# Optimization experiments

Measured on AMD Instinct MI355X. Metric: run time of the kernel, lower is better.

## Reference

```python
import jax, jax.numpy as jnp
import numpy as np

N, IN_DIM, H1, H2 = 12288, 512, 256, 128

def setup_inputs() -> dict:
    key = jax.random.key(0)
    k = jax.random.split(key, 6)
    glorot = lambda kk, fi, fo: jax.random.normal(kk, (fi, fo), jnp.float32) * np.sqrt(2.0 / (fi + fo))
    return {
        "X": jax.random.normal(k[0], (N, IN_DIM), jnp.float32),
        "adj": jax.random.uniform(k[1], (N, N), jnp.float32) / N,  # scaled like a normalized adjacency
        "noise": jax.random.normal(k[2], (N, H2), jnp.float32),
        "W0": glorot(k[3], IN_DIM, H1),
        "W_mu": glorot(k[4], H1, H2),
        "W_logstd": glorot(k[5], H1, H2),
    }

def reference(X, adj, noise, W0, W_mu, W_logstd):
    # GraphConvSparse layer 1: relu(adj @ (X @ W0))
    hidden = jax.nn.relu(adj @ (X @ W0))            # [N, H1]
    # mean / logstd heads (identity activation)
    mean = adj @ (hidden @ W_mu)                    # [N, H2]
    logstd = adj @ (hidden @ W_logstd)              # [N, H2]
    # reparameterization
    Z = noise * jnp.exp(logstd) + mean              # [N, H2]
    # dot-product decode
    A_pred = jax.nn.sigmoid(Z @ Z.T)                # [N, N]
    return A_pred
```

## Files before the change

kernel.cpp:

```cpp
#include <hip/hip_runtime.h>
#include <hip/hip_fp8.h>
#include <stdint.h>

#define NN 12288
#define IND 512
#define H1D 256
#define H2D 128

using bf16x8 = __attribute__((ext_vector_type(8))) short;
using f32x4  = __attribute__((ext_vector_type(4))) float;
using u32x4  = __attribute__((ext_vector_type(4))) unsigned int;

__device__ __forceinline__ unsigned short f2bf(float f){
  unsigned int u = __float_as_uint(f);
  return (unsigned short)((u + 0x7fffu + ((u >> 16) & 1u)) >> 16);
}
__device__ __forceinline__ float bf2f(unsigned short h){
  return __uint_as_float(((unsigned int)h) << 16);
}
__device__ __forceinline__ void gload_lds16(const void* g, void* l){
  __builtin_amdgcn_global_load_lds(
      (const __attribute__((address_space(1))) unsigned int*)(uintptr_t)g,
      (__attribute__((address_space(3))) unsigned int*)(unsigned int)(uintptr_t)l,
      16, 0, 0);
}
template<bool HI>
__device__ __forceinline__ unsigned cvt2(float a, float b, unsigned old){
#if __has_builtin(__builtin_amdgcn_cvt_pk_fp8_f32)
  return (unsigned)__builtin_amdgcn_cvt_pk_fp8_f32(a, b, (int)old, HI);
#else
  __hip_fp8_e4m3 pa(a), pb(b);
  unsigned v = (unsigned)pa.__x | ((unsigned)pb.__x << 8);
  return HI ? ((old & 0x0000FFFFu) | (v << 16)) : ((old & 0xFFFF0000u) | v);
#endif
}
__device__ __forceinline__ void sync_v(int n){
  switch(n){
    case 0: asm volatile("s_waitcnt vmcnt(0) lgkmcnt(0)" ::: "memory"); break;
    case 1: asm volatile("s_waitcnt vmcnt(1) lgkmcnt(0)" ::: "memory"); break;
    case 4: asm volatile("s_waitcnt vmcnt(4) lgkmcnt(0)" ::: "memory"); break;
    default: asm volatile("s_waitcnt vmcnt(5) lgkmcnt(0)" ::: "memory"); break;
  }
  __builtin_amdgcn_s_barrier();
  __builtin_amdgcn_sched_barrier(0);
}

__global__ __launch_bounds__(256) void k_w0t(const float* __restrict__ W0,
                                             char* __restrict__ W0T){
  __shared__ float Ls[64][65];
  const int t = (int)threadIdx.x;
  const int k0 = (int)blockIdx.x * 64;
  const int h0 = (int)blockIdx.y * 64;
  {
    const int r = t >> 2, c = (t & 3) * 16;
    const float* p = W0 + (size_t)(k0 + r) * H1D + h0 + c;
#pragma unroll
    for (int q = 0; q < 4; ++q)
      *(float4*)&Ls[r][c + q*4] = *(const float4*)(p + q*4);
  }
  __syncthreads();
  const int h = t >> 2, kc = (t & 3) * 16;
  u32x4 pk;
#pragma unroll
  for (int q = 0; q < 4; ++q){
    unsigned wv = cvt2<false>(Ls[kc+q*4+0][h], Ls[kc+q*4+1][h], 0u);
    wv = cvt2<true>(Ls[kc+q*4+2][h], Ls[kc+q*4+3][h], wv);
    pk[q] = wv;
  }
  *(u32x4*)(W0T + (size_t)(h0 + h) * IND + k0 + kc) = pk;
}

#define GEMM_MFMA_F8(CUR) \
  { _Pragma("unroll") \
    for (int kk = 0; kk < 4; ++kk){ \
      long af[3]; long bfr[2]; \
      _Pragma("unroll") \
      for (int mi = 0; mi < 3; ++mi){ \
        int row = mi*16 + l15; \
        int off = row*128 + ((kk*32 + l16*8) ^ ((row & 7) << 4)); \
        af[mi] = *(const long*)(Alds[CUR] + off); \
      } \
      _Pragma("unroll") \
      for (int ni = 0; ni < 2; ++ni){ \
        int row = w*32 + ni*16 + l15; \
        int off = row*128 + ((kk*32 + l16*8) ^ ((row & 7) << 4)); \
        bfr[ni] = *(const long*)(Blds[CUR] + off); \
      } \
      _Pragma("unroll") \
      for (int mi = 0; mi < 3; ++mi) \
        _Pragma("unroll") \
        for (int ni = 0; ni < 2; ++ni) \
          acc[mi][ni] = __builtin_amdgcn_mfma_f32_16x16x32_fp8_fp8(af[mi], bfr[ni], acc[mi][ni], 0, 0, 0); \
    } }

#define GLDS_B(SIDX, BUF) \
  { _Pragma("unroll") \
    for (int i = 0; i < 4; ++i){ \
      int P = i*8192 + t*16; \
      int row = P >> 7; \
      int Li = (P & 127) ^ ((row & 7) << 4); \
      gload_lds16(btb + (size_t)row * btsb + kbB + (size_t)(SIDX)*128 + Li, \
                  Blds[BUF] + i*8192 + w*1024); \
    } }

#define GLDS_A(SIDX, BUF) \
  if (w < 6){ \
    gload_lds16(af8 + (size_t)(m0 + w*8 + rw8) * NN + kbase + (size_t)(SIDX)*128 + gsw, \
                Alds[BUF] + w*1024); \
  }

#define LOAD_A(Q0,Q1,Q2,Q3, SIDX) { \
  const float* p = abase + (size_t)(SIDX)*128; \
  Q0 = __builtin_nontemporal_load((const f32x4*)(p)); \
  Q1 = __builtin_nontemporal_load((const f32x4*)(p+4)); \
  Q2 = __builtin_nontemporal_load((const f32x4*)(p+8)); \
  Q3 = __builtin_nontemporal_load((const f32x4*)(p+12)); \
}

#define PACK_A(Q0,Q1,Q2,Q3, BUF, SIDX) { \
  u32x4 pk; \
  pk[0] = cvt2<false>(Q0[0]*ascale, Q0[1]*ascale, 0u); pk[0] = cvt2<true>(Q0[2]*ascale, Q0[3]*ascale, pk[0]); \
  pk[1] = cvt2<false>(Q1[0]*ascale, Q1[1]*ascale, 0u); pk[1] = cvt2<true>(Q1[2]*ascale, Q1[3]*ascale, pk[1]); \
  pk[2] = cvt2<false>(Q2[0]*ascale, Q2[1]*ascale, 0u); pk[2] = cvt2<true>(Q2[2]*ascale, Q2[3]*ascale, pk[2]); \
  pk[3] = cvt2<false>(Q3[0]*ascale, Q3[1]*ascale, 0u); pk[3] = cvt2<true>(Q3[2]*ascale, Q3[3]*ascale, pk[3]); \
  *(u32x4*)(Alds[BUF] + aoff) = pk; \
  if (DUMP) __builtin_nontemporal_store(pk, (u32x4*)(dumpP + (size_t)(m0 + ar) * NN + kbase + (size_t)(SIDX)*128 + ac)); \
}

template<int AMODE, int MODE, int DUMP>
__global__ __launch_bounds__(512, 4) void k_gemm_f8(const void* __restrict__ Ain, int lda, int K,
                                                    const char* __restrict__ Bt, int bt_stride_b,
                                                    float ascale, char* __restrict__ dumpP,
                                                    void* __restrict__ Out){
  __shared__ __align__(16) char Alds[2][48*128];
  __shared__ __align__(16) char Blds[2][256*128];
  const int t = (int)threadIdx.x;
  const int w = t >> 6, l = t & 63;
  const int l15 = l & 15, l16 = l >> 4;

  int midx, khalf;
  if (gridDim.x == 512){
    int f = (int)blockIdx.x;
    int x = f & 7;
    khalf = x >> 2;
    midx = (f >> 3) * 4 + (x & 3);
  } else { khalf = 0; midx = (int)blockIdx.x; }
  const int m0 = midx * 48;
  const int kbase = khalf * K;
  const size_t kbB = (size_t)kbase;
  const size_t btsb = (size_t)bt_stride_b;
  const char* btb = Bt;
  const int S = K >> 7;

  f32x4 acc[3][2];
#pragma unroll
  for (int mi = 0; mi < 3; ++mi)
#pragma unroll
    for (int ni = 0; ni < 2; ++ni) acc[mi][ni] = 0;

  const int ar = t >> 3, ac = (t & 7) * 16;
  const bool astage = (w < 6);
  const float* abase = (const float*)Ain + (size_t)(m0 + ar) * lda + kbase + ac;
  const int aoff = ar*128 + (ac ^ ((ar & 7) << 4));
  const char* af8 = (const char*)Ain;
  const int rw8 = l >> 3;
  const int gsw = ((l & 7) ^ rw8) << 4;

  if (AMODE == 0){
    f32x4 s0q0, s0q1, s0q2, s0q3, s1q0, s1q1, s1q2, s1q3;
    GLDS_B(0, 0);
    if (astage){
      LOAD_A(s0q0,s0q1,s0q2,s0q3, 0);
      if (S > 1) LOAD_A(s1q0,s1q1,s1q2,s1q3, 1);
      PACK_A(s0q0,s0q1,s0q2,s0q3, 0, 0);
    }
    sync_v(astage ? (DUMP ? 5 : 4) : 0);

    for (int s = 0; s < S; s += 2){
      if (s + 1 < S) GLDS_B(s + 1, 1);
      if (astage && s + 2 < S) LOAD_A(s0q0,s0q1,s0q2,s0q3, s + 2);
      GEMM_MFMA_F8(0);
      if (astage && s + 1 < S) PACK_A(s1q0,s1q1,s1q2,s1q3, 1, s + 1);
      if (s + 1 < S)
        sync_v(astage ? ((s + 2 < S) ? (DUMP ? 5 : 4) : (DUMP ? 1 : 0)) : 0);
      if (s + 1 < S){
        if (s + 2 < S) GLDS_B(s + 2, 0);
        if (astage && s + 3 < S) LOAD_A(s1q0,s1q1,s1q2,s1q3, s + 3);
        GEMM_MFMA_F8(1);
        if (astage && s + 2 < S) PACK_A(s0q0,s0q1,s0q2,s0q3, 0, s + 2);
        if (s + 2 < S)
          sync_v(astage ? ((s + 3 < S) ? (DUMP ? 5 : 4) : (DUMP ? 1 : 0)) : 0);
      }
    }
  } else {
    GLDS_B(0, 0);
    GLDS_A(0, 0);
    sync_v(0);
    for (int s = 0; s < S; ++s){
      const int cur = s & 1, nxt = cur ^ 1;
      if (s + 1 < S){ GLDS_B(s + 1, nxt); GLDS_A(s + 1, nxt); }
      if (cur == 0){ GEMM_MFMA_F8(0); } else { GEMM_MFMA_F8(1); }
      if (s + 1 < S) sync_v(0);
    }
  }

  if (MODE == 0){
    char* OutT = (char*)Out;
#pragma unroll
    for (int mi = 0; mi < 3; ++mi)
#pragma unroll
      for (int ni = 0; ni < 2; ++ni){
        int gr = m0 + mi*16 + l16*4;
        int gc = w*32 + ni*16 + l15;
        unsigned wd = cvt2<false>(acc[mi][ni][0], acc[mi][ni][1], 0u);
        wd = cvt2<true>(acc[mi][ni][2], acc[mi][ni][3], wd);
        *(unsigned*)(OutT + (size_t)gc * NN + gr) = wd;
      }
  } else {
    float* P = (float*)Out + (size_t)khalf * NN * H1D;
#pragma unroll
    for (int mi = 0; mi < 3; ++mi)
#pragma unroll
      for (int ni = 0; ni < 2; ++ni){
        int gr = m0 + mi*16 + l16*4;
        int gc = w*32 + ni*16 + l15;
#pragma unroll
        for (int v = 0; v < 4; ++v)
          P[(size_t)(gr + v) * H1D + gc] = acc[mi][ni][v];
      }
  }
}

__global__ __launch_bounds__(256) void k_combine_ht(const float* __restrict__ p0,
                                                    const float* __restrict__ p1,
                                                    char* __restrict__ HT){
  __shared__ float Ls[64][65];
  const int t = (int)threadIdx.x;
  const int n0 = (int)blockIdx.x * 64;
  const int h0 = (int)blockIdx.y * 64;
  const int lr = t >> 4, lc = (t & 15) * 4;
#pragma unroll
  for (int q = 0; q < 4; ++q){
    int n = lr + q*16;
    size_t idx = (size_t)(n0 + n) * H1D + h0 + lc;
    float4 a = *(const float4*)(p0 + idx);
    float4 b = *(const float4*)(p1 + idx);
    Ls[n][lc+0] = fmaxf(a.x + b.x, 0.f);
    Ls[n][lc+1] = fmaxf(a.y + b.y, 0.f);
    Ls[n][lc+2] = fmaxf(a.z + b.z, 0.f);
    Ls[n][lc+3] = fmaxf(a.w + b.w, 0.f);
  }
  __syncthreads();
  const int hr = t >> 2, nc = (t & 3) * 16;
  u32x4 pk;
#pragma unroll
  for (int q = 0; q < 4; ++q){
    unsigned wd = cvt2<false>(Ls[nc+q*4+0][hr], Ls[nc+q*4+1][hr], 0u);
    wd = cvt2<true>(Ls[nc+q*4+2][hr], Ls[nc+q*4+3][hr], wd);
    pk[q] = wd;
  }
  *(u32x4*)(HT + (size_t)(h0 + hr) * NN + n0 + nc) = pk;
}

__global__ __launch_bounds__(256) void k_heads(const float* __restrict__ p0,
                                               const float* __restrict__ Wmu,
                                               const float* __restrict__ Wls,
                                               const float* __restrict__ noise,
                                               unsigned short* __restrict__ Zhi,
                                               unsigned short* __restrict__ Zlo){
  __shared__ float AHs[32][256];
  __shared__ float Wms[32][128];
  __shared__ float Wlss[32][128];
  const float INV = 1.0f / 67108864.0f;
  const float* p1 = p0 + (size_t)NN * H1D;
  const int t  = (int)threadIdx.x;
  const int r0 = (int)blockIdx.x * 32;
  {
    const int r = t >> 3, c0 = (t & 7) * 32;
    size_t base = (size_t)(r0 + r) * H1D + c0;
#pragma unroll
    for (int q = 0; q < 8; ++q){
      float4 a = *(const float4*)(p0 + base + q*4);
      float4 b = *(const float4*)(p1 + base + q*4);
      AHs[r][c0 + q*4 + 0] = (a.x + b.x) * INV;
      AHs[r][c0 + q*4 + 1] = (a.y + b.y) * INV;
      AHs[r][c0 + q*4 + 2] = (a.z + b.z) * INV;
      AHs[r][c0 + q*4 + 3] = (a.w + b.w) * INV;
    }
  }
  const int j = t & 127, rg = t >> 7;
  float mu[16], ls[16];
#pragma unroll
  for (int r = 0; r < 16; ++r){ mu[r] = 0.f; ls[r] = 0.f; }

  for (int kc = 0; kc < 8; ++kc){
    __syncthreads();
    {
      const int r = t >> 3, c0 = (t & 7) * 16;
      const float* pm = Wmu + (size_t)(kc*32 + r) * H2D + c0;
      const float* pl = Wls + (size_t)(kc*32 + r) * H2D + c0;
#pragma unroll
      for (int q = 0; q < 4; ++q){
        *(float4*)&Wms[r][c0 + q*4]  = *(const float4*)(pm + q*4);
        *(float4*)&Wlss[r][c0 + q*4] = *(const float4*)(pl + q*4);
      }
    }
    __syncthreads();
#pragma unroll 4
    for (int k = 0; k < 32; ++k){
      float wm = Wms[k][j], wl = Wlss[k][j];
#pragma unroll
      for (int r = 0; r < 16; ++r){
        float a = AHs[rg*16 + r][kc*32 + k];
        mu[r] += a * wm;
        ls[r] += a * wl;
      }
    }
  }
#pragma unroll
  for (int r = 0; r < 16; ++r){
    const int i = r0 + rg*16 + r;
    float z = noise[(size_t)i * H2D + j] * __expf(ls[r]) + mu[r];
    unsigned short zh = f2bf(z);
    unsigned short zl = f2bf(z - bf2f(zh));
    Zhi[(size_t)i * H2D + j] = zh;
    Zlo[(size_t)i * H2D + j] = zl;
  }
}

__global__ __launch_bounds__(512) void k_decode(const unsigned short* __restrict__ Zhi,
                                                const unsigned short* __restrict__ Zlo,
                                                float* __restrict__ Out){
  __shared__ unsigned short T[4][128*64];
  const int t = (int)threadIdx.x;
  const int w = t >> 6, l = t & 63;
  const int l15 = l & 15, l16 = l >> 4;
  const int wr = w >> 2, wc = w & 3;
  const size_t m0 = (size_t)blockIdx.x * 128;
  const size_t n0 = (size_t)blockIdx.y * 128;

  f32x4 acc[4][2];
#pragma unroll
  for (int mi = 0; mi < 4; ++mi)
#pragma unroll
    for (int ni = 0; ni < 2; ++ni) acc[mi][ni] = 0;

#pragma unroll
  for (int p = 0; p < 2; ++p){
    if (p) __syncthreads();
#pragma unroll
    for (int i = 0; i < 2; ++i){
      int P = i*8192 + t*16;
      int row = P >> 7;
      int Li = (P & 127) ^ ((row & 7) << 4);
      size_t ga = (size_t)row * 256 + (size_t)p * 128 + Li;
      char* lb0 = (char*)T[0] + i*8192 + w*1024;
      char* lb1 = (char*)T[1] + i*8192 + w*1024;
      char* lb2 = (char*)T[2] + i*8192 + w*1024;
      char* lb3 = (char*)T[3] + i*8192 + w*1024;
      gload_lds16((const char*)Zhi + m0*256 + ga, lb0);
      gload_lds16((const char*)Zlo + m0*256 + ga, lb1);
      gload_lds16((const char*)Zhi + n0*256 + ga, lb2);
      gload_lds16((const char*)Zlo + n0*256 + ga, lb3);
    }
    __syncthreads();
#pragma unroll
    for (int kk = 0; kk < 2; ++kk){
      bf16x8 ah[4], al[4], bh[2], bl[2];
#pragma unroll
      for (int mi = 0; mi < 4; ++mi){
        int row = wr*64 + mi*16 + l15;
        int off = row*128 + ((kk*64 + l16*16) ^ ((row & 7) << 4));
        ah[mi] = *(const bf16x8*)((const char*)T[0] + off);
        al[mi] = *(const bf16x8*)((const char*)T[1] + off);
      }
#pragma unroll
      for (int ni = 0; ni < 2; ++ni){
        int row = wc*32 + ni*16 + l15;
        int off = row*128 + ((kk*64 + l16*16) ^ ((row & 7) << 4));
        bh[ni] = *(const bf16x8*)((const char*)T[2] + off);
        bl[ni] = *(const bf16x8*)((const char*)T[3] + off);
      }
#pragma unroll
      for (int mi = 0; mi < 4; ++mi)
#pragma unroll
        for (int ni = 0; ni < 2; ++ni){
          acc[mi][ni] = __builtin_amdgcn_mfma_f32_16x16x32_bf16(ah[mi], bh[ni], acc[mi][ni], 0, 0, 0);
          acc[mi][ni] = __builtin_amdgcn_mfma_f32_16x16x32_bf16(ah[mi], bl[ni], acc[mi][ni], 0, 0, 0);
          acc[mi][ni] = __builtin_amdgcn_mfma_f32_16x16x32_bf16(al[mi], bh[ni], acc[mi][ni], 0, 0, 0);
        }
    }
  }

#pragma unroll
  for (int mi = 0; mi < 4; ++mi)
#pragma unroll
    for (int ni = 0; ni < 2; ++ni){
      size_t gr = m0 + (size_t)(wr*64 + mi*16 + l16*4);
      size_t gc = n0 + (size_t)(wc*32 + ni*16 + l15);
#pragma unroll
      for (int v = 0; v < 4; ++v){
        float x = acc[mi][ni][v];
        float sg = 1.0f / (1.0f + __expf(-x));
        __builtin_nontemporal_store(sg, &Out[(gr + v) * (size_t)NN + gc]);
      }
    }
}

extern "C" void kernel_launch(void* const* d_in, const int* in_sizes, int n_in,
                              void* d_out, int out_size, void* d_ws, size_t ws_size,
                              hipStream_t stream) {
  const float* X     = (const float*)d_in[0];
  const float* adj   = (const float*)d_in[1];
  const float* noise = (const float*)d_in[2];
  const float* W0    = (const float*)d_in[3];
  const float* Wmu   = (const float*)d_in[4];
  const float* Wls   = (const float*)d_in[5];
  float* out = (float*)d_out;
  char* ws = (char*)d_ws;

  char*           XW0Tf8 = ws;
  char*           HidTf8 = ws + 3145728;
  char*           W0Tf8  = ws + 6291456;
  unsigned short* Zhi    = (unsigned short*)(ws + 6422528);
  unsigned short* Zlo    = (unsigned short*)(ws + 9568256);
  char*  adjf8 = (char*)d_out;
  float* part  = (float*)((char*)d_out + 150994944);

  const float S_ADJ = 8192.0f;

  k_w0t<<<dim3(8, 4), 256, 0, stream>>>(W0, W0Tf8);
  k_gemm_f8<0,0,0><<<256, 512, 0, stream>>>((const void*)X, IND, IND, W0Tf8, IND, 1.0f, nullptr, (void*)XW0Tf8);
  k_gemm_f8<0,1,1><<<512, 512, 0, stream>>>((const void*)adj, NN, 6144, XW0Tf8, NN, S_ADJ, adjf8, (void*)part);
  k_combine_ht<<<dim3(192, 4), 256, 0, stream>>>(part, part + (size_t)NN * H1D, HidTf8);
  k_gemm_f8<1,1,0><<<512, 512, 0, stream>>>((const void*)adjf8, NN, 6144, HidTf8, NN, 1.0f, nullptr, (void*)part);
  k_heads<<<384, 256, 0, stream>>>(part, Wmu, Wls, noise, Zhi, Zlo);
  k_decode<<<dim3(96, 96), 512, 0, stream>>>(Zhi, Zlo, out);
}
```

Before: 627.7 us.

## Split fp32-to-fp8 conversion into standalone kernels and unify GEMM into one fp8 kernel

Moves the fp32-to-fp8 conversion of adj and X out of the GEMM mainloop into a separate grid-stride conversion kernel. The GEMM then becomes a single simpler fp8 kernel with 256 threads and a 64x128 tile, split in N, where all operands are staged with global_load_lds. This removes the in-register conversion and the dump path from the first adjacency GEMM, at the cost of an extra full pass over the 600MB adj before that GEMM. It may also change occupancy and tile efficiency.

```diff
diff --git a/kernel.cpp b/kernel.cpp
--- a/kernel.cpp
+++ b/kernel.cpp
@@ -34,15 +34,29 @@
   return HI ? ((old & 0x0000FFFFu) | (v << 16)) : ((old & 0xFFFF0000u) | v);
 #endif
 }
-__device__ __forceinline__ void sync_v(int n){
-  switch(n){
-    case 0: asm volatile("s_waitcnt vmcnt(0) lgkmcnt(0)" ::: "memory"); break;
-    case 1: asm volatile("s_waitcnt vmcnt(1) lgkmcnt(0)" ::: "memory"); break;
-    case 4: asm volatile("s_waitcnt vmcnt(4) lgkmcnt(0)" ::: "memory"); break;
-    default: asm volatile("s_waitcnt vmcnt(5) lgkmcnt(0)" ::: "memory"); break;
-  }
+__device__ __forceinline__ void sync0(){
+  asm volatile("s_waitcnt vmcnt(0) lgkmcnt(0)" ::: "memory");
   __builtin_amdgcn_s_barrier();
   __builtin_amdgcn_sched_barrier(0);
+}
+
+__global__ __launch_bounds__(256) void k_cvt(const float* __restrict__ in,
+                                             char* __restrict__ out,
+                                             float scale, long n16){
+  const long stride = (long)gridDim.x * 256;
+  for (long i = (long)blockIdx.x * 256 + threadIdx.x; i < n16; i += stride){
+    const f32x4* p = (const f32x4*)(in + i * 16);
+    f32x4 a = __builtin_nontemporal_load(p);
+    f32x4 b = __builtin_nontemporal_load(p + 1);
+    f32x4 c = __builtin_nontemporal_load(p + 2);
+    f32x4 d = __builtin_nontemporal_load(p + 3);
+    u32x4 pk;
+    pk[0] = cvt2<false>(a[0]*scale, a[1]*scale, 0u); pk[0] = cvt2<true>(a[2]*scale, a[3]*scale, pk[0]);
+    pk[1] = cvt2<false>(b[0]*scale, b[1]*scale, 0u); pk[1] = cvt2<true>(b[2]*scale, b[3]*scale, pk[1]);
+    pk[2] = cvt2<false>(c[0]*scale, c[1]*scale, 0u); pk[2] = cvt2<true>(c[2]*scale, c[3]*scale, pk[2]);
+    pk[3] = cvt2<false>(d[0]*scale, d[1]*scale, 0u); pk[3] = cvt2<true>(d[2]*scale, d[3]*scale, pk[3]);
+    *(u32x4*)(out + i * 16) = pk;
+  }
 }
 
 __global__ __launch_bounds__(256) void k_w0t(const float* __restrict__ W0,
@@ -70,148 +84,88 @@
   *(u32x4*)(W0T + (size_t)(h0 + h) * IND + k0 + kc) = pk;
 }
 
-#define GEMM_MFMA_F8(CUR) \
-  { _Pragma("unroll") \
-    for (int kk = 0; kk < 4; ++kk){ \
-      long af[3]; long bfr[2]; \
+#define STAGE(BUF, SIDX) { \
+  _Pragma("unroll") \
+  for (int p = 0; p < 2; ++p) \
+    gload_lds16(Ap + (size_t)(p*32) * lda + (size_t)(SIDX)*128, \
+                Alds[BUF] + p*4096 + w*1024); \
+  _Pragma("unroll") \
+  for (int i = 0; i < 4; ++i) \
+    gload_lds16(Bp + (size_t)(i*32) * ldb + (size_t)(SIDX)*128, \
+                Blds[BUF] + i*4096 + w*1024); \
+}
+
+#define MF8(CUR) { \
+  _Pragma("unroll") \
+  for (int kk = 0; kk < 4; ++kk){ \
+    long af[4]; long bfr[2]; \
+    _Pragma("unroll") \
+    for (int mi = 0; mi < 4; ++mi){ \
+      int row = mi*16 + l15; \
+      int off = row*128 + ((kk*32 + l16*8) ^ ((row & 7) << 4)); \
+      af[mi] = *(const long*)(Alds[CUR] + off); \
+    } \
+    _Pragma("unroll") \
+    for (int ni = 0; ni < 2; ++ni){ \
+      int row = w*32 + ni*16 + l15; \
+      int off = row*128 + ((kk*32 + l16*8) ^ ((row & 7) << 4)); \
+      bfr[ni] = *(const long*)(Blds[CUR] + off); \
+    } \
+    _Pragma("unroll") \
+    for (int mi = 0; mi < 4; ++mi) \
       _Pragma("unroll") \
-      for (int mi = 0; mi < 3; ++mi){ \
-        int row = mi*16 + l15; \
-        int off = row*128 + ((kk*32 + l16*8) ^ ((row & 7) << 4)); \
-        af[mi] = *(const long*)(Alds[CUR] + off); \
-      } \
-      _Pragma("unroll") \
-      for (int ni = 0; ni < 2; ++ni){ \
-        int row = w*32 + ni*16 + l15; \
-        int off = row*128 + ((kk*32 + l16*8) ^ ((row & 7) << 4)); \
-        bfr[ni] = *(const long*)(Blds[CUR] + off); \
-      } \
-      _Pragma("unroll") \
-      for (int mi = 0; mi < 3; ++mi) \
-        _Pragma("unroll") \
-        for (int ni = 0; ni < 2; ++ni) \
-          acc[mi][ni] = __builtin_amdgcn_mfma_f32_16x16x32_fp8_fp8(af[mi], bfr[ni], acc[mi][ni], 0, 0, 0); \
-    } }
-
-#define GLDS_B(SIDX, BUF) \
-  { _Pragma("unroll") \
-    for (int i = 0; i < 4; ++i){ \
-      int P = i*8192 + t*16; \
-      int row = P >> 7; \
-      int Li = (P & 127) ^ ((row & 7) << 4); \
-      gload_lds16(btb + (size_t)row * btsb + kbB + (size_t)(SIDX)*128 + Li, \
-                  Blds[BUF] + i*8192 + w*1024); \
-    } }
-
-#define GLDS_A(SIDX, BUF) \
-  if (w < 6){ \
-    gload_lds16(af8 + (size_t)(m0 + w*8 + rw8) * NN + kbase + (size_t)(SIDX)*128 + gsw, \
-                Alds[BUF] + w*1024); \
-  }
-
-#define LOAD_A(Q0,Q1,Q2,Q3, SIDX) { \
-  const float* p = abase + (size_t)(SIDX)*128; \
-  Q0 = __builtin_nontemporal_load((const f32x4*)(p)); \
-  Q1 = __builtin_nontemporal_load((const f32x4*)(p+4)); \
-  Q2 = __builtin_nontemporal_load((const f32x4*)(p+8)); \
-  Q3 = __builtin_nontemporal_load((const f32x4*)(p+12)); \
-}
-
-#define PACK_A(Q0,Q1,Q2,Q3, BUF, SIDX) { \
-  u32x4 pk; \
-  pk[0] = cvt2<false>(Q0[0]*ascale, Q0[1]*ascale, 0u); pk[0] = cvt2<true>(Q0[2]*ascale, Q0[3]*ascale, pk[0]); \
-  pk[1] = cvt2<false>(Q1[0]*ascale, Q1[1]*ascale, 0u); pk[1] = cvt2<true>(Q1[2]*ascale, Q1[3]*ascale, pk[1]); \
-  pk[2] = cvt2<false>(Q2[0]*ascale, Q2[1]*ascale, 0u); pk[2] = cvt2<true>(Q2[2]*ascale, Q2[3]*ascale, pk[2]); \
-  pk[3] = cvt2<false>(Q3[0]*ascale, Q3[1]*ascale, 0u); pk[3] = cvt2<true>(Q3[2]*ascale, Q3[3]*ascale, pk[3]); \
-  *(u32x4*)(Alds[BUF] + aoff) = pk; \
-  if (DUMP) __builtin_nontemporal_store(pk, (u32x4*)(dumpP + (size_t)(m0 + ar) * NN + kbase + (size_t)(SIDX)*128 + ac)); \
-}
-
-template<int AMODE, int MODE, int DUMP>
-__global__ __launch_bounds__(512, 4) void k_gemm_f8(const void* __restrict__ Ain, int lda, int K,
-                                                    const char* __restrict__ Bt, int bt_stride_b,
-                                                    float ascale, char* __restrict__ dumpP,
-                                                    void* __restrict__ Out){
-  __shared__ __align__(16) char Alds[2][48*128];
-  __shared__ __align__(16) char Blds[2][256*128];
+      for (int ni = 0; ni < 2; ++ni) \
+        acc[mi][ni] = __builtin_amdgcn_mfma_f32_16x16x32_fp8_fp8(af[mi], bfr[ni], acc[mi][ni], 0, 0, 0); \
+  } }
+
+template<int KSPLIT, int MODE>
+__global__ __launch_bounds__(256, 3) void k_gf8(const char* __restrict__ A, int lda, int K,
+                                                const char* __restrict__ Bt, int ldb,
+                                                void* __restrict__ Out){
+  __shared__ __align__(16) char Alds[2][64*128];
+  __shared__ __align__(16) char Blds[2][128*128];
   const int t = (int)threadIdx.x;
   const int w = t >> 6, l = t & 63;
   const int l15 = l & 15, l16 = l >> 4;
 
-  int midx, khalf;
-  if (gridDim.x == 512){
-    int f = (int)blockIdx.x;
-    int x = f & 7;
+  int khalf, idx;
+  if (KSPLIT == 2){
+    int f = (int)blockIdx.x, x = f & 7;
     khalf = x >> 2;
-    midx = (f >> 3) * 4 + (x & 3);
-  } else { khalf = 0; midx = (int)blockIdx.x; }
-  const int m0 = midx * 48;
-  const int kbase = khalf * K;
-  const size_t kbB = (size_t)kbase;
-  const size_t btsb = (size_t)bt_stride_b;
-  const char* btb = Bt;
+    idx = (f >> 3) * 4 + (x & 3);
+  } else { khalf = 0; idx = (int)blockIdx.x; }
+  const int m0 = (idx >> 1) * 64;
+  const int nh = idx & 1;
+  const size_t kb = (size_t)khalf * K;
   const int S = K >> 7;
 
-  f32x4 acc[3][2];
-#pragma unroll
-  for (int mi = 0; mi < 3; ++mi)
+  f32x4 acc[4][2];
+#pragma unroll
+  for (int mi = 0; mi < 4; ++mi)
 #pragma unroll
     for (int ni = 0; ni < 2; ++ni) acc[mi][ni] = 0;
 
-  const int ar = t >> 3, ac = (t & 7) * 16;
-  const bool astage = (w < 6);
-  const float* abase = (const float*)Ain + (size_t)(m0 + ar) * lda + kbase + ac;
-  const int aoff = ar*128 + (ac ^ ((ar & 7) << 4));
-  const char* af8 = (const char*)Ain;
-  const int rw8 = l >> 3;
-  const int gsw = ((l & 7) ^ rw8) << 4;
-
-  if (AMODE == 0){
-    f32x4 s0q0, s0q1, s0q2, s0q3, s1q0, s1q1, s1q2, s1q3;
-    GLDS_B(0, 0);
-    if (astage){
-      LOAD_A(s0q0,s0q1,s0q2,s0q3, 0);
-      if (S > 1) LOAD_A(s1q0,s1q1,s1q2,s1q3, 1);
-      PACK_A(s0q0,s0q1,s0q2,s0q3, 0, 0);
-    }
-    sync_v(astage ? (DUMP ? 5 : 4) : 0);
-
-    for (int s = 0; s < S; s += 2){
-      if (s + 1 < S) GLDS_B(s + 1, 1);
-      if (astage && s + 2 < S) LOAD_A(s0q0,s0q1,s0q2,s0q3, s + 2);
-      GEMM_MFMA_F8(0);
-      if (astage && s + 1 < S) PACK_A(s1q0,s1q1,s1q2,s1q3, 1, s + 1);
-      if (s + 1 < S)
-        sync_v(astage ? ((s + 2 < S) ? (DUMP ? 5 : 4) : (DUMP ? 1 : 0)) : 0);
-      if (s + 1 < S){
-        if (s + 2 < S) GLDS_B(s + 2, 0);
-        if (astage && s + 3 < S) LOAD_A(s1q0,s1q1,s1q2,s1q3, s + 3);
-        GEMM_MFMA_F8(1);
-        if (astage && s + 2 < S) PACK_A(s0q0,s0q1,s0q2,s0q3, 0, s + 2);
-        if (s + 2 < S)
-          sync_v(astage ? ((s + 3 < S) ? (DUMP ? 5 : 4) : (DUMP ? 1 : 0)) : 0);
-      }
-    }
-  } else {
-    GLDS_B(0, 0);
-    GLDS_A(0, 0);
-    sync_v(0);
-    for (int s = 0; s < S; ++s){
-      const int cur = s & 1, nxt = cur ^ 1;
-      if (s + 1 < S){ GLDS_B(s + 1, nxt); GLDS_A(s + 1, nxt); }
-      if (cur == 0){ GEMM_MFMA_F8(0); } else { GEMM_MFMA_F8(1); }
-      if (s + 1 < S) sync_v(0);
-    }
+  const int swz = ((l & 7) ^ (l >> 3)) << 4;
+  const char* Ap = A  + (size_t)(m0 + w*8 + (l >> 3)) * lda + kb + swz;
+  const char* Bp = Bt + (size_t)(nh*128 + w*8 + (l >> 3)) * ldb + kb + swz;
+
+  STAGE(0, 0);
+  sync0();
+  for (int s = 0; s < S; ++s){
+    const int cur = s & 1;
+    if (s + 1 < S){ if (cur == 0){ STAGE(1, s + 1); } else { STAGE(0, s + 1); } }
+    if (cur == 0){ MF8(0); } else { MF8(1); }
+    if (s + 1 < S) sync0();
   }
 
   if (MODE == 0){
     char* OutT = (char*)Out;
 #pragma unroll
-    for (int mi = 0; mi < 3; ++mi)
+    for (int mi = 0; mi < 4; ++mi)
 #pragma unroll
       for (int ni = 0; ni < 2; ++ni){
         int gr = m0 + mi*16 + l16*4;
-        int gc = w*32 + ni*16 + l15;
+        int gc = nh*128 + w*32 + ni*16 + l15;
         unsigned wd = cvt2<false>(acc[mi][ni][0], acc[mi][ni][1], 0u);
         wd = cvt2<true>(acc[mi][ni][2], acc[mi][ni][3], wd);
         *(unsigned*)(OutT + (size_t)gc * NN + gr) = wd;
@@ -219,11 +173,11 @@
   } else {
     float* P = (float*)Out + (size_t)khalf * NN * H1D;
 #pragma unroll
-    for (int mi = 0; mi < 3; ++mi)
+    for (int mi = 0; mi < 4; ++mi)
 #pragma unroll
       for (int ni = 0; ni < 2; ++ni){
         int gr = m0 + mi*16 + l16*4;
-        int gc = w*32 + ni*16 + l15;
+        int gc = nh*128 + w*32 + ni*16 + l15;
 #pragma unroll
         for (int v = 0; v < 4; ++v)
           P[(size_t)(gr + v) * H1D + gc] = acc[mi][ni][v];
@@ -424,16 +378,19 @@
   char*           W0Tf8  = ws + 6291456;
   unsigned short* Zhi    = (unsigned short*)(ws + 6422528);
   unsigned short* Zlo    = (unsigned short*)(ws + 9568256);
+  char*           Xf8    = ws + 12713984;
   char*  adjf8 = (char*)d_out;
   float* part  = (float*)((char*)d_out + 150994944);
 
   const float S_ADJ = 8192.0f;
 
+  k_cvt<<<2048, 256, 0, stream>>>(adj, adjf8, S_ADJ, (long)NN * NN / 16);
   k_w0t<<<dim3(8, 4), 256, 0, stream>>>(W0, W0Tf8);
-  k_gemm_f8<0,0,0><<<256, 512, 0, stream>>>((const void*)X, IND, IND, W0Tf8, IND, 1.0f, nullptr, (void*)XW0Tf8);
-  k_gemm_f8<0,1,1><<<512, 512, 0, stream>>>((const void*)adj, NN, 6144, XW0Tf8, NN, S_ADJ, adjf8, (void*)part);
+  k_cvt<<<256, 256, 0, stream>>>(X, Xf8, 1.0f, (long)NN * IND / 16);
+  k_gf8<1,0><<<384, 256, 0, stream>>>(Xf8, IND, IND, W0Tf8, IND, (void*)XW0Tf8);
+  k_gf8<2,1><<<768, 256, 0, stream>>>(adjf8, NN, 6144, XW0Tf8, NN, (void*)part);
   k_combine_ht<<<dim3(192, 4), 256, 0, stream>>>(part, part + (size_t)NN * H1D, HidTf8);
-  k_gemm_f8<1,1,0><<<512, 512, 0, stream>>>((const void*)adjf8, NN, 6144, HidTf8, NN, 1.0f, nullptr, (void*)part);
+  k_gf8<2,1><<<768, 256, 0, stream>>>(adjf8, NN, 6144, HidTf8, NN, (void*)part);
   k_heads<<<384, 256, 0, stream>>>(part, Wmu, Wls, noise, Zhi, Zlo);
   k_decode<<<dim3(96, 96), 512, 0, stream>>>(Zhi, Zlo, out);
 }
```

New measurement: 616.6 us. No clear change (-1.8%).
